# Performance work log

Hardware: AMD Instinct MI355X
Metric: run time of the kernel (lower is better)

Reference implementation:

```python
import jax, jax.numpy as jnp
import numpy as np

H = 64  # GRU hidden size


def _gru_layer(x, Wih, Whh, bih, bhh):
    """PyTorch-semantics GRU layer. x: [B,T,I] -> [B,T,H].
    r = sig(Wir x + bir + Whr h + bhr); z = sig(...); n = tanh(Win x + bin + r*(Whn h + bhn))
    h' = (1-z)*n + z*h. Gate order in stacked weights: r, z, n."""
    xg = jnp.einsum('bti,gi->btg', x, Wih) + bih  # [B,T,3H], precomputed input projections

    def step(h, xg_t):
        hg = h @ Whh.T + bhh  # [B,3H]
        xr, xz, xn = jnp.split(xg_t, 3, axis=-1)
        hr, hz, hn = jnp.split(hg, 3, axis=-1)
        r = jax.nn.sigmoid(xr + hr)
        z = jax.nn.sigmoid(xz + hz)
        n = jnp.tanh(xn + r * hn)
        h_new = (1.0 - z) * n + z * h
        return h_new, h_new

    h0 = jnp.zeros((x.shape[0], H), x.dtype)
    _, ys = jax.lax.scan(step, h0, jnp.swapaxes(xg, 0, 1))  # scan over time
    return jnp.swapaxes(ys, 0, 1)  # [B,T,H]


def _gru_stack4(x, Wih0, Wih, Whh, bih, bhh):
    # layer 0 has its own input width; layers 1..3 take H->H. Inter-layer dropout
    # (p=0.2) is inference-disabled.
    y = _gru_layer(x, Wih0, Whh[0], bih[0], bhh[0])
    for l in range(3):
        y = _gru_layer(y, Wih[l], Whh[l + 1], bih[l + 1], bhh[l + 1])
    return y


def _bn_eval(x, gamma, beta, mean, var, eps=1e-5):
    return gamma * (x - mean) * jax.lax.rsqrt(var + eps) + beta


def setup_inputs() -> dict:
    key = jax.random.key(0)
    ks = jax.random.split(key, 32)
    B, T = 2048, 256
    d = {}
    d['sentiment_seq'] = jax.random.normal(ks[0], (B, T), jnp.float32)
    d['price_seq'] = jax.random.normal(ks[1], (B, T, 4), jnp.float32)
    w = lambda k, s: jax.random.normal(k, s, jnp.float32) * 0.1
    d['s_Wih0'] = w(ks[2], (192, 1)); d['s_Wih'] = w(ks[3], (3, 192, 64))
    d['s_Whh'] = w(ks[4], (4, 192, 64)); d['s_bih'] = w(ks[5], (4, 192)); d['s_bhh'] = w(ks[6], (4, 192))
    d['p_Wih0'] = w(ks[7], (192, 4)); d['p_Wih'] = w(ks[8], (3, 192, 64))
    d['p_Whh'] = w(ks[9], (4, 192, 64)); d['p_bih'] = w(ks[10], (4, 192)); d['p_bhh'] = w(ks[11], (4, 192))
    d['fc1_W'] = w(ks[12], (128, 128)); d['fc1_b'] = w(ks[13], (128,))
    d['bn1_gamma'] = jax.random.uniform(ks[14], (128,), jnp.float32, 0.5, 1.5)
    d['bn1_beta'] = w(ks[15], (128,)); d['bn1_mean'] = w(ks[16], (128,))
    d['bn1_var'] = jax.random.uniform(ks[17], (128,), jnp.float32, 0.5, 1.5)
    d['fc2_W'] = w(ks[18], (128, 128)); d['fc2_b'] = w(ks[19], (128,))
    d['bn2_gamma'] = jax.random.uniform(ks[20], (128,), jnp.float32, 0.5, 1.5)
    d['bn2_beta'] = w(ks[21], (128,)); d['bn2_mean'] = w(ks[22], (128,))
    d['bn2_var'] = jax.random.uniform(ks[23], (128,), jnp.float32, 0.5, 1.5)
    d['fc3_W'] = w(ks[24], (2, 128)); d['fc3_b'] = w(ks[25], (2,))
    return d


def reference(sentiment_seq, price_seq,
              s_Wih0, s_Wih, s_Whh, s_bih, s_bhh,
              p_Wih0, p_Wih, p_Whh, p_bih, p_bhh,
              fc1_W, fc1_b, bn1_gamma, bn1_beta, bn1_mean, bn1_var,
              fc2_W, fc2_b, bn2_gamma, bn2_beta, bn2_mean, bn2_var,
              fc3_W, fc3_b):
    # input_size[0] == 1 -> unsqueeze last dim (as in the torch module)
    s = sentiment_seq[..., None]                         # [B,T,1]
    s_out = _gru_stack4(s, s_Wih0, s_Wih, s_Whh, s_bih, s_bhh)
    p_out = _gru_stack4(price_seq, p_Wih0, p_Wih, p_Whh, p_bih, p_bhh)
    x = jnp.concatenate([s_out[:, -1, :], p_out[:, -1, :]], axis=1)  # [B,128]
    x = x @ fc1_W.T + fc1_b
    x = jax.nn.relu(_bn_eval(x, bn1_gamma, bn1_beta, bn1_mean, bn1_var))  # dropout off (eval)
    x = x @ fc2_W.T + fc2_b
    x = jax.nn.relu(_bn_eval(x, bn2_gamma, bn2_beta, bn2_mean, bn2_var))
    return x @ fc3_W.T + fc3_b  # [B,2] logits
```

## Files before the change

kernel.cpp:

```cpp
#include <hip/hip_runtime.h>

namespace {

constexpr int BB = 2048;
constexpr int TT = 256;
constexpr float L2E = 1.4426950408889634f;

typedef __attribute__((ext_vector_type(8))) short bf8;
typedef __attribute__((ext_vector_type(4))) float f4;
typedef __attribute__((ext_vector_type(2))) unsigned int u32x2;

#define MFMA16(a, b, c) __builtin_amdgcn_mfma_f32_16x16x32_bf16((a), (b), (c), 0, 0, 0)

__device__ __forceinline__ unsigned short f2bf_rne(float f) {
  unsigned int x = __float_as_uint(f);
  return (unsigned short)((x + 0x7fffu + ((x >> 16) & 1u)) >> 16);
}
__device__ __forceinline__ void mk_hilo(float v, short& hi, short& lo) {
  unsigned int u = __float_as_uint(v);
  hi = (short)(u >> 16);
  float r = v - __uint_as_float(u & 0xffff0000u);
  lo = (short)(__float_as_uint(r) >> 16);
}

__global__ __launch_bounds__(1024, 4) void gru_all(
    const float* __restrict__ xs, const float* __restrict__ xp,
    const float* __restrict__ W0s, const float* __restrict__ W0p,
    const float* __restrict__ Wihs, const float* __restrict__ Wihp,
    const float* __restrict__ Whhs, const float* __restrict__ Whhp,
    const float* __restrict__ bihs, const float* __restrict__ bihp,
    const float* __restrict__ bhhs, const float* __restrict__ bhhp,
    float* __restrict__ hlast) {
  const int tid = threadIdx.x;
  const int Wv = tid >> 6, lane = tid & 63;
  const int g = Wv >> 2, w = Wv & 3;
  const int n15 = lane & 15, q = lane >> 4;
  const int blk = blockIdx.x, stack = blk >> 7;
  const int b0 = (blk & 127) * 16;

  const float* Wh = (stack ? Whhp : Whhs) + (size_t)g * 192 * 64;
  const float* bi = (stack ? bihp : bihs) + g * 192;
  const float* bh = (stack ? bhhp : bhhs) + g * 192;
  const float* Wx = (stack ? Wihp : Wihs) + (size_t)(g - 1) * 192 * 64;

  __shared__ unsigned short hb[4][4][8][16][8];

  for (int e = tid; e < 4 * 4 * 8 * 16 * 8; e += 1024)
    ((unsigned short*)hb)[e] = 0;

  const int mrow = 16 * w + n15;
  const int mu = 16 * w + 4 * q;
  const int fr_w = 2 * w + (q >> 1);
  const int eo_w = (q & 1) * 4;

  const float gsc[3] = {L2E, L2E, 2.f * L2E};

  bf8 whh_[3][2];
  #pragma unroll
  for (int i = 0; i < 3; ++i) {
    #pragma unroll
    for (int kt = 0; kt < 2; ++kt) {
      const float* ph_ = Wh + (size_t)(i * 64 + mrow) * 64 + kt * 32 + q * 8;
      f4 ha = *(const f4*)ph_, hc = *(const f4*)(ph_ + 4);
      bf8 h2;
      #pragma unroll
      for (int j = 0; j < 8; ++j)
        h2[j] = (short)f2bf_rne(gsc[i] * ((j < 4) ? ha[j] : hc[j - 4]));
      whh_[i][kt] = h2;
    }
  }
  bf8 wxh_[3][2];
  if (g >= 1) {
    #pragma unroll
    for (int i = 0; i < 3; ++i) {
      #pragma unroll
      for (int kt = 0; kt < 2; ++kt) {
        const float* px_ = Wx + (size_t)(i * 64 + mrow) * 64 + kt * 32 + q * 8;
        f4 xa = *(const f4*)px_, xc = *(const f4*)(px_ + 4);
        bf8 h1;
        #pragma unroll
        for (int j = 0; j < 8; ++j)
          h1[j] = (short)f2bf_rne(gsc[i] * ((j < 4) ? xa[j] : xc[j - 4]));
        wxh_[i][kt] = h1;
      }
    }
  } else {
    const float* W0 = stack ? W0p : W0s;
    #pragma unroll
    for (int i = 0; i < 3; ++i) {
      bf8 a;
      #pragma unroll
      for (int j = 0; j < 8; ++j) a[j] = 0;
      if (q == 0) {
        if (stack) {
          #pragma unroll
          for (int d = 0; d < 4; ++d) {
            short hi, lo;
            mk_hilo(gsc[i] * W0[(size_t)(i * 64 + mrow) * 4 + d], hi, lo);
            a[d] = hi; a[4 + d] = lo;
          }
        } else {
          short hi, lo; mk_hilo(gsc[i] * W0[i * 64 + mrow], hi, lo);
          a[0] = hi; a[1] = hi; a[4] = lo; a[5] = lo;
        }
      }
      wxh_[i][0] = a; wxh_[i][1] = a;
    }
  }

  f4 bR, bZ, bNx, bNh;
  #pragma unroll
  for (int r = 0; r < 4; ++r) {
    bR[r]  = L2E * (bi[mu + r] + bh[mu + r]);
    bZ[r]  = L2E * (bi[64 + mu + r] + bh[64 + mu + r]);
    bNx[r] = 2.f * L2E * bi[128 + mu + r];
    bNh[r] = 2.f * L2E * bh[128 + mu + r];
  }
  f4 h = {0.f, 0.f, 0.f, 0.f};

  const unsigned short* rs0[4];
  const unsigned short* rp0[4];
  unsigned short* ws0[4];
  #pragma unroll
  for (int j = 0; j < 4; ++j) {
    const int s_self = (j - g) & 3;
    const int s_next = (j - g + 1) & 3;
    rs0[j] = &hb[g][s_self][q][n15][0];
    ws0[j] = &hb[g][s_next][fr_w][n15][eo_w];
    rp0[j] = &hb[(g >= 1 ? g - 1 : 0)][s_next][q][n15][0];
  }

  const size_t xrow = (size_t)(b0 + n15);
  float px0 = 0.f, px1 = 0.f, px2 = 0.f, px3 = 0.f;
  if (g == 0) {
    if (stack) { f4 t4 = *(const f4*)(xp + xrow * TT * 4); px0 = t4[0]; px1 = t4[1]; px2 = t4[2]; px3 = t4[3]; }
    else       { px0 = xs[xrow * TT]; }
  }
  __syncthreads();

#define GRU_BODY(S)                                                            \
  {                                                                            \
    const int tc = s + S - g;                                                  \
    if ((unsigned)tc < (unsigned)TT) {                                         \
      f4 aR = bR, aZ = bZ, aNx = bNx, aNh = bNh;                               \
      bf8 hh0 = *(const bf8*)rs0[S];                                           \
      bf8 hh1 = *(const bf8*)(rs0[S] + 512);                                   \
      if (g == 0) {                                                            \
        bf8 xq;                                                                \
        _Pragma("unroll") for (int j = 0; j < 8; ++j) xq[j] = 0;               \
        if (q == 0) {                                                          \
          if (stack) {                                                         \
            short a0 = (short)f2bf_rne(px0), a1 = (short)f2bf_rne(px1);        \
            short a2 = (short)f2bf_rne(px2), a3 = (short)f2bf_rne(px3);        \
            xq[0] = a0; xq[1] = a1; xq[2] = a2; xq[3] = a3;                    \
            xq[4] = a0; xq[5] = a1; xq[6] = a2; xq[7] = a3;                    \
          } else {                                                             \
            unsigned short xh = f2bf_rne(px0);                                 \
            float xf = __uint_as_float((unsigned)xh << 16);                    \
            unsigned short xl = f2bf_rne(px0 - xf);                            \
            xq[0] = (short)xh; xq[1] = (short)xl;                              \
            xq[4] = (short)xh; xq[5] = (short)xl;                              \
          }                                                                    \
        }                                                                      \
        __builtin_amdgcn_s_setprio(1);                                         \
        aR  = MFMA16(wxh_[0][0], xq, aR);                                      \
        aZ  = MFMA16(wxh_[1][0], xq, aZ);                                      \
        aNx = MFMA16(wxh_[2][0], xq, aNx);                                     \
        aR  = MFMA16(whh_[0][0], hh0, aR);  aR  = MFMA16(whh_[0][1], hh1, aR); \
        aZ  = MFMA16(whh_[1][0], hh0, aZ);  aZ  = MFMA16(whh_[1][1], hh1, aZ); \
        aNh = MFMA16(whh_[2][0], hh0, aNh); aNh = MFMA16(whh_[2][1], hh1, aNh);\
        __builtin_amdgcn_s_setprio(0);                                         \
        if (tc + 1 < TT) {                                                     \
          if (stack) { f4 t4 = *(const f4*)(xp + (xrow * TT + tc + 1) * 4);    \
                       px0 = t4[0]; px1 = t4[1]; px2 = t4[2]; px3 = t4[3]; }   \
          else       { px0 = xs[xrow * TT + tc + 1]; }                         \
        }                                                                      \
      } else {                                                                 \
        bf8 xc0 = *(const bf8*)rp0[S];                                         \
        bf8 xc1 = *(const bf8*)(rp0[S] + 512);                                 \
        __builtin_amdgcn_s_setprio(1);                                         \
        aR  = MFMA16(wxh_[0][0], xc0, aR);  aR  = MFMA16(wxh_[0][1], xc1, aR); \
        aZ  = MFMA16(wxh_[1][0], xc0, aZ);  aZ  = MFMA16(wxh_[1][1], xc1, aZ); \
        aNx = MFMA16(wxh_[2][0], xc0, aNx); aNx = MFMA16(wxh_[2][1], xc1, aNx);\
        aR  = MFMA16(whh_[0][0], hh0, aR);  aR  = MFMA16(whh_[0][1], hh1, aR); \
        aZ  = MFMA16(whh_[1][0], hh0, aZ);  aZ  = MFMA16(whh_[1][1], hh1, aZ); \
        aNh = MFMA16(whh_[2][0], hh0, aNh); aNh = MFMA16(whh_[2][1], hh1, aNh);\
        __builtin_amdgcn_s_setprio(0);                                         \
      }                                                                        \
      _Pragma("unroll") for (int r = 0; r < 4; ++r) {                          \
        float eR = __builtin_amdgcn_exp2f(-aR[r]);                             \
        float eZ = __builtin_amdgcn_exp2f(-aZ[r]);                             \
        float dR = 1.f + eR, dZ = 1.f + eZ;                                    \
        float qq = __builtin_amdgcn_rcpf(dR * dZ);                             \
        float rr = dZ * qq;                                   \
        float zz = dR * qq;                                   \
        float eN = __builtin_amdgcn_exp2f(aNx[r] + rr * aNh[r]);               \
        float nn = 1.f - 2.f * __builtin_amdgcn_rcpf(eN + 1.f);                \
        h[r] = nn + zz * (h[r] - nn);                                          \
      }                                                                        \
      unsigned p01, p23;                                                       \
      asm("v_cvt_pk_bf16_f32 %0, %1, %2" : "=v"(p01) : "v"(h[0]), "v"(h[1])); \
      asm("v_cvt_pk_bf16_f32 %0, %1, %2" : "=v"(p23) : "v"(h[2]), "v"(h[3])); \
      u32x2 hiw = {p01, p23};                                                  \
      *(u32x2*)ws0[S] = hiw;                                                   \
      if (g == 3 && tc == TT - 1)                                              \
        *(f4*)&hlast[((size_t)stack * BB + b0 + n15) * 64 + mu] = h;           \
    }                                                                          \
    __syncthreads();                                                           \
  }

  for (int s = 0; s < TT + 4; s += 4) {
    GRU_BODY(0)
    GRU_BODY(1)
    GRU_BODY(2)
    GRU_BODY(3)
  }
#undef GRU_BODY
}

__global__ __launch_bounds__(128) void head(
    const float* __restrict__ hlast,
    const float* __restrict__ W1, const float* __restrict__ b1,
    const float* __restrict__ g1, const float* __restrict__ be1,
    const float* __restrict__ m1, const float* __restrict__ v1,
    const float* __restrict__ W2, const float* __restrict__ b2,
    const float* __restrict__ g2, const float* __restrict__ be2,
    const float* __restrict__ m2, const float* __restrict__ v2,
    const float* __restrict__ W3, const float* __restrict__ b3,
    float* __restrict__ out) {
  const int b = blockIdx.x;
  const int j = threadIdx.x;
  __shared__ float xin[128];
  __shared__ float y1[128];
  __shared__ float y2[128];
  xin[j] = (j < 64) ? hlast[(size_t)b * 64 + j]
                    : hlast[(size_t)BB * 64 + (size_t)b * 64 + (j - 64)];
  __syncthreads();
  float acc = b1[j];
  #pragma unroll 8
  for (int k = 0; k < 128; ++k) acc = fmaf(W1[j * 128 + k], xin[k], acc);
  float sc = g1[j] * rsqrtf(v1[j] + 1e-5f);
  y1[j] = fmaxf(0.f, (acc - m1[j]) * sc + be1[j]);
  __syncthreads();
  acc = b2[j];
  #pragma unroll 8
  for (int k = 0; k < 128; ++k) acc = fmaf(W2[j * 128 + k], y1[k], acc);
  sc = g2[j] * rsqrtf(v2[j] + 1e-5f);
  y2[j] = fmaxf(0.f, (acc - m2[j]) * sc + be2[j]);
  __syncthreads();
  if (j < 2) {
    float a = b3[j];
    #pragma unroll 8
    for (int k = 0; k < 128; ++k) a = fmaf(W3[j * 128 + k], y2[k], a);
    out[(size_t)b * 2 + j] = a;
  }
}

}

extern "C" void kernel_launch(void* const* d_in, const int* in_sizes, int n_in,
                              void* d_out, int out_size, void* d_ws, size_t ws_size,
                              hipStream_t stream) {
  (void)in_sizes; (void)n_in; (void)out_size; (void)ws_size;
  const float* sent   = (const float*)d_in[0];
  const float* price  = (const float*)d_in[1];
  const float* s_Wih0 = (const float*)d_in[2];
  const float* s_Wih  = (const float*)d_in[3];
  const float* s_Whh  = (const float*)d_in[4];
  const float* s_bih  = (const float*)d_in[5];
  const float* s_bhh  = (const float*)d_in[6];
  const float* p_Wih0 = (const float*)d_in[7];
  const float* p_Wih  = (const float*)d_in[8];
  const float* p_Whh  = (const float*)d_in[9];
  const float* p_bih  = (const float*)d_in[10];
  const float* p_bhh  = (const float*)d_in[11];
  const float* fc1_W  = (const float*)d_in[12];
  const float* fc1_b  = (const float*)d_in[13];
  const float* bn1_g  = (const float*)d_in[14];
  const float* bn1_b  = (const float*)d_in[15];
  const float* bn1_m  = (const float*)d_in[16];
  const float* bn1_v  = (const float*)d_in[17];
  const float* fc2_W  = (const float*)d_in[18];
  const float* fc2_b  = (const float*)d_in[19];
  const float* bn2_g  = (const float*)d_in[20];
  const float* bn2_b  = (const float*)d_in[21];
  const float* bn2_m  = (const float*)d_in[22];
  const float* bn2_v  = (const float*)d_in[23];
  const float* fc3_W  = (const float*)d_in[24];
  const float* fc3_b  = (const float*)d_in[25];
  float* out = (float*)d_out;

  float* hlast = (float*)d_ws;

  gru_all<<<dim3(256), dim3(1024), 0, stream>>>(
      sent, price, s_Wih0, p_Wih0, s_Wih, p_Wih, s_Whh, p_Whh,
      s_bih, p_bih, s_bhh, p_bhh, hlast);

  head<<<dim3(BB), dim3(128), 0, stream>>>(
      hlast, fc1_W, fc1_b, bn1_g, bn1_b, bn1_m, bn1_v,
      fc2_W, fc2_b, bn2_g, bn2_b, bn2_m, bn2_v, fc3_W, fc3_b, out);
}
```

Before: 283.7 us.

## Prefetch previous-layer outputs one step ahead and peel wavefront loop guards

The layer wavefront skew changes from one step to two steps per layer. Each upper layer can then read its input from the previous layer's hidden buffer at the end of the prior step, into registers, before the barrier, which takes that LDS load off the critical path ahead of the MFMAs. The main time loop is split into a guarded prologue, an unguarded steady-state body and a guarded epilogue to remove per-step bounds checks. The cost is extra pipeline fill and drain steps and more live registers, and the ring-buffer slot indexing must stay correct under the new skew.

Result: slower. 291.0 us (+2.6%).

```diff
diff --git a/kernel.cpp b/kernel.cpp
--- a/kernel.cpp
+++ b/kernel.cpp
@@ -119,15 +119,13 @@
   f4 h = {0.f, 0.f, 0.f, 0.f};
 
   const unsigned short* rs0[4];
+  unsigned short* ws0[4];
   const unsigned short* rp0[4];
-  unsigned short* ws0[4];
   #pragma unroll
   for (int j = 0; j < 4; ++j) {
-    const int s_self = (j - g) & 3;
-    const int s_next = (j - g + 1) & 3;
-    rs0[j] = &hb[g][s_self][q][n15][0];
-    ws0[j] = &hb[g][s_next][fr_w][n15][eo_w];
-    rp0[j] = &hb[(g >= 1 ? g - 1 : 0)][s_next][q][n15][0];
+    rs0[j] = &hb[g][(j - 2 * g) & 3][q][n15][0];
+    ws0[j] = &hb[g][(j - 2 * g + 1) & 3][fr_w][n15][eo_w];
+    rp0[j] = &hb[(g >= 1 ? g - 1 : 0)][(j - 2 * g + 2) & 3][q][n15][0];
   }
 
   const size_t xrow = (size_t)(b0 + n15);
@@ -136,15 +134,16 @@
     if (stack) { f4 t4 = *(const f4*)(xp + xrow * TT * 4); px0 = t4[0]; px1 = t4[1]; px2 = t4[2]; px3 = t4[3]; }
     else       { px0 = xs[xrow * TT]; }
   }
+  bf8 xpf0 = {}, xpf1 = {};
   __syncthreads();
 
-#define GRU_BODY(S)                                                            \
+#define GRU_STEP(S, GD)                                                        \
   {                                                                            \
-    const int tc = s + S - g;                                                  \
-    if ((unsigned)tc < (unsigned)TT) {                                         \
-      f4 aR = bR, aZ = bZ, aNx = bNx, aNh = bNh;                               \
+    const int tc = s + (S) - 2 * g;                                            \
+    if (!(GD) || (unsigned)tc < (unsigned)TT) {                                \
       bf8 hh0 = *(const bf8*)rs0[S];                                           \
       bf8 hh1 = *(const bf8*)(rs0[S] + 512);                                   \
+      f4 aR = bR, aZ = bZ, aNx = bNx, aNh = bNh;                               \
       if (g == 0) {                                                            \
         bf8 xq;                                                                \
         _Pragma("unroll") for (int j = 0; j < 8; ++j) xq[j] = 0;               \
@@ -170,18 +169,17 @@
         aZ  = MFMA16(whh_[1][0], hh0, aZ);  aZ  = MFMA16(whh_[1][1], hh1, aZ); \
         aNh = MFMA16(whh_[2][0], hh0, aNh); aNh = MFMA16(whh_[2][1], hh1, aNh);\
         __builtin_amdgcn_s_setprio(0);                                         \
-        if (tc + 1 < TT) {                                                     \
+        if (!(GD) || tc + 1 < TT) {                                            \
           if (stack) { f4 t4 = *(const f4*)(xp + (xrow * TT + tc + 1) * 4);    \
                        px0 = t4[0]; px1 = t4[1]; px2 = t4[2]; px3 = t4[3]; }   \
           else       { px0 = xs[xrow * TT + tc + 1]; }                         \
         }                                                                      \
       } else {                                                                 \
-        bf8 xc0 = *(const bf8*)rp0[S];                                         \
-        bf8 xc1 = *(const bf8*)(rp0[S] + 512);                                 \
+           \
         __builtin_amdgcn_s_setprio(1);                                         \
-        aR  = MFMA16(wxh_[0][0], xc0, aR);  aR  = MFMA16(wxh_[0][1], xc1, aR); \
-        aZ  = MFMA16(wxh_[1][0], xc0, aZ);  aZ  = MFMA16(wxh_[1][1], xc1, aZ); \
-        aNx = MFMA16(wxh_[2][0], xc0, aNx); aNx = MFMA16(wxh_[2][1], xc1, aNx);\
+        aR  = MFMA16(wxh_[0][0], xpf0, aR);  aR  = MFMA16(wxh_[0][1], xpf1, aR);  \
+        aZ  = MFMA16(wxh_[1][0], xpf0, aZ);  aZ  = MFMA16(wxh_[1][1], xpf1, aZ);  \
+        aNx = MFMA16(wxh_[2][0], xpf0, aNx); aNx = MFMA16(wxh_[2][1], xpf1, aNx); \
         aR  = MFMA16(whh_[0][0], hh0, aR);  aR  = MFMA16(whh_[0][1], hh1, aR); \
         aZ  = MFMA16(whh_[1][0], hh0, aZ);  aZ  = MFMA16(whh_[1][1], hh1, aZ); \
         aNh = MFMA16(whh_[2][0], hh0, aNh); aNh = MFMA16(whh_[2][1], hh1, aNh);\
@@ -206,16 +204,26 @@
       if (g == 3 && tc == TT - 1)                                              \
         *(f4*)&hlast[((size_t)stack * BB + b0 + n15) * 64 + mu] = h;           \
     }                                                                          \
+    if (g >= 1) {                                                              \
+      const int tn_ = s + (S) - 2 * g + 1;                                     \
+      if (!(GD) || (unsigned)tn_ < (unsigned)TT) {                             \
+        xpf0 = *(const bf8*)rp0[S];                                            \
+        xpf1 = *(const bf8*)(rp0[S] + 512);                                    \
+      }                                                                        \
+    }                                                                          \
     __syncthreads();                                                           \
   }
 
-  for (int s = 0; s < TT + 4; s += 4) {
-    GRU_BODY(0)
-    GRU_BODY(1)
-    GRU_BODY(2)
-    GRU_BODY(3)
-  }
-#undef GRU_BODY
+  for (int s = 0; s < 8; s += 4) {
+    GRU_STEP(0, 1) GRU_STEP(1, 1) GRU_STEP(2, 1) GRU_STEP(3, 1)
+  }
+  for (int s = 8; s < 252; s += 4) {
+    GRU_STEP(0, 0) GRU_STEP(1, 0) GRU_STEP(2, 0) GRU_STEP(3, 0)
+  }
+  for (int s = 252; s < 264; s += 4) {
+    GRU_STEP(0, 1) GRU_STEP(1, 1) GRU_STEP(2, 1) GRU_STEP(3, 1)
+  }
+#undef GRU_STEP
 }
 
 __global__ __launch_bounds__(128) void head(
```
